# Kernel optimization log

Hardware: AMD Instinct MI355X
Metric: run time of the kernel (lower is better)

Reference implementation:

```python
import jax, jax.numpy as jnp
import numpy as np

H = 16          # local heads
DN = 128        # qk_nope_head_dim
DR = 64         # qk_rope_head_dim
DV = 128        # v_head_dim
QL = 1536       # q_lora_rank
KVL = 512       # kv_lora_rank
HID = 5120      # hidden_size
T = 2048        # tokens
EPS = 1e-6
THETA = 10000.0
SCALE = (DN + DR) ** -0.5


def rmsnorm(x, w):
    return x * jax.lax.rsqrt(jnp.mean(x * x, axis=-1, keepdims=True) + EPS) * w


def rope_interleaved(x, pos):
    # non-neox (GPT-J interleaved) partial RoPE on last dim DR; x: [T, h, DR]
    inv_freq = 1.0 / (THETA ** (jnp.arange(0, DR, 2, dtype=jnp.float32) / DR))
    freqs = pos[:, None].astype(jnp.float32) * inv_freq          # [T, DR/2]
    cos = jnp.cos(freqs)[:, None, :]
    sin = jnp.sin(freqs)[:, None, :]
    x1, x2 = x[..., 0::2], x[..., 1::2]
    o1 = x1 * cos - x2 * sin
    o2 = x2 * cos + x1 * sin
    return jnp.stack([o1, o2], axis=-1).reshape(x.shape)


def setup_inputs() -> dict:
    key = jax.random.key(0)
    ks = jax.random.split(key, 8)
    s = lambda d: 1.0 / np.sqrt(d)
    return {
        "positions": jnp.arange(T, dtype=jnp.int64),
        "hidden_states": jax.random.normal(ks[0], (T, HID), jnp.float32),
        "wq_a": jax.random.normal(ks[1], (HID, QL), jnp.float32) * s(HID),
        "q_a_ln": jnp.ones((QL,), jnp.float32),
        "wq_b": jax.random.normal(ks[2], (QL, H * (DN + DR)), jnp.float32) * s(QL),
        "wkv_a": jax.random.normal(ks[3], (HID, KVL + DR), jnp.float32) * s(HID),
        "kv_a_ln": jnp.ones((KVL,), jnp.float32),
        "wkv_b": jax.random.normal(ks[4], (KVL, H * (DN + DV)), jnp.float32) * s(KVL),
        "wo": jax.random.normal(ks[5], (H * DV, HID), jnp.float32) * s(H * DV),
    }


def reference(positions, hidden_states, wq_a, q_a_ln, wq_b, wkv_a, kv_a_ln, wkv_b, wo):
    Tn = hidden_states.shape[0]
    # Q path: low-rank down, RMSNorm, up to per-head qk dims
    q = rmsnorm(hidden_states @ wq_a, q_a_ln) @ wq_b            # [T, H*(DN+DR)]
    q = q.reshape(Tn, H, DN + DR)
    q_nope, q_pe = q[..., :DN], q[..., DN:]
    # KV path: joint down-projection -> latent + shared rope key
    kv = hidden_states @ wkv_a                                   # [T, KVL+DR]
    c_kv, k_pe = kv[:, :KVL], kv[:, KVL:]
    c_kv = rmsnorm(c_kv, kv_a_ln)
    kvb = (c_kv @ wkv_b).reshape(Tn, H, DN + DV)
    k_nope, v = kvb[..., :DN], kvb[..., DN:]
    # partial RoPE on rope sub-dims only
    q_pe = rope_interleaved(q_pe, positions)                     # [T, H, DR]
    k_pe = rope_interleaved(k_pe[:, None, :], positions)         # [T, 1, DR]
    # causal attention over full qk_head_dim
    scores = (jnp.einsum('thd,shd->hts', q_nope, k_nope)
              + jnp.einsum('thd,sod->hts', q_pe, k_pe)) * SCALE  # [H, T, T]
    mask = jnp.tril(jnp.ones((Tn, Tn), bool))
    scores = jnp.where(mask[None], scores, jnp.finfo(scores.dtype).min)
    attn = jax.nn.softmax(scores, axis=-1)
    out = jnp.einsum('hts,shd->thd', attn, v).reshape(Tn, H * DV)
    return out @ wo                                              # [T, HID]
```

## Files before the change

### kernel.cpp

```cpp
#include <hip/hip_runtime.h>
#include <hip/hip_bf16.h>


typedef __attribute__((ext_vector_type(8))) short bf16x8;
typedef __attribute__((ext_vector_type(4))) float f32x4;

#define T_SEQ 2048
#define NH 16
#define DNOPE 128
#define DROPE 64
#define DVAL 128
#define QLORA 1536
#define KVLORA 512
#define HID 5120
#define ATTN_SCALE 0.07216878364870323f

static __device__ __forceinline__ float bf2f(__hip_bfloat16 b) { return __bfloat162float(b); }

__global__ void cvt_kernel(const float* __restrict__ in, __hip_bfloat16* __restrict__ out, int n) {
  for (int i = (blockIdx.x * 256 + threadIdx.x) * 4; i < n; i += gridDim.x * 256 * 4) {
    float4 v = *(const float4*)(in + i);
    out[i + 0] = __float2bfloat16(v.x);
    out[i + 1] = __float2bfloat16(v.y);
    out[i + 2] = __float2bfloat16(v.z);
    out[i + 3] = __float2bfloat16(v.w);
  }
}

__global__ void transpose_cvt_kernel(const float* __restrict__ in, __hip_bfloat16* __restrict__ out,
                                     int R, int C) {
  __shared__ float tile[32][33];
  int bi = blockIdx.x, bj = blockIdx.y;
  int tx = threadIdx.x & 31, ty = threadIdx.x >> 5;
#pragma unroll
  for (int k2 = 0; k2 < 4; k2++) {
    int r = bi * 32 + ty + k2 * 8;
    tile[ty + k2 * 8][tx] = in[(size_t)r * C + bj * 32 + tx];
  }
  __syncthreads();
#pragma unroll
  for (int k2 = 0; k2 < 4; k2++) {
    int cc = bj * 32 + ty + k2 * 8;
    out[(size_t)cc * R + bi * 32 + tx] = __float2bfloat16(tile[tx][ty + k2 * 8]);
  }
}

__global__ void rmsnorm_kernel(const float* __restrict__ in, int in_stride, int cols,
                               const float* __restrict__ wgt,
                               __hip_bfloat16* __restrict__ out, int out_stride) {
  int row = blockIdx.x;
  const float* x = in + (size_t)row * in_stride;
  float ss = 0.f;
  for (int c = threadIdx.x; c < cols; c += 256) { float v = x[c]; ss += v * v; }
#pragma unroll
  for (int d = 1; d < 64; d <<= 1) ss += __shfl_xor(ss, d, 64);
  __shared__ float red[4];
  if ((threadIdx.x & 63) == 0) red[threadIdx.x >> 6] = ss;
  __syncthreads();
  float tot = red[0] + red[1] + red[2] + red[3];
  float r = rsqrtf(tot / cols + 1e-6f);
  __hip_bfloat16* o = out + (size_t)row * out_stride;
  for (int c = threadIdx.x; c < cols; c += 256)
    o[c] = __float2bfloat16(x[c] * r * wgt[c]);
}

__global__ void rope_q_kernel(__hip_bfloat16* __restrict__ q) {
  int row = blockIdx.x;
#pragma unroll
  for (int jj = 0; jj < 2; jj++) {
    int v = threadIdx.x + 256 * jj;
    int h = v >> 5, i = v & 31;
    float inv = powf(10000.f, -(2.f * i) / 64.f);
    float fr = (float)row * inv;
    float s, c;
    sincosf(fr, &s, &c);
    __hip_bfloat16* p = q + (size_t)row * 3072 + h * 192 + 128 + 2 * i;
    float x1 = bf2f(p[0]), x2 = bf2f(p[1]);
    p[0] = __float2bfloat16(x1 * c - x2 * s);
    p[1] = __float2bfloat16(x2 * c + x1 * s);
  }
}

__global__ void rope_k_kernel(const float* __restrict__ kv, __hip_bfloat16* __restrict__ kpe) {
  int row = blockIdx.x;
  int i = threadIdx.x;
  if (i < 32) {
    float inv = powf(10000.f, -(2.f * i) / 64.f);
    float fr = (float)row * inv;
    float s, c;
    sincosf(fr, &s, &c);
    float x1 = kv[(size_t)row * 576 + 512 + 2 * i];
    float x2 = kv[(size_t)row * 576 + 513 + 2 * i];
    kpe[(size_t)row * 64 + 2 * i]     = __float2bfloat16(x1 * c - x2 * s);
    kpe[(size_t)row * 64 + 2 * i + 1] = __float2bfloat16(x2 * c + x1 * s);
  }
}

#define BT_PAD 40
template <bool OUT_BF16>
__global__ __launch_bounds__(256, 2) void gemm_bt_kernel(
    const __hip_bfloat16* __restrict__ A, const __hip_bfloat16* __restrict__ Bt,
    void* __restrict__ Cout, int M, int N, int K) {
  __shared__ __hip_bfloat16 As[2][128][BT_PAD];
  __shared__ __hip_bfloat16 Bs[2][128][BT_PAD];
  const int t = threadIdx.x;
  const int w = t >> 6, l = t & 63;
  const int lr = l & 15, lh = l >> 4;
  const int wr = w >> 1, wc = w & 1;
  const int bm = blockIdx.x, bn = blockIdx.y;

  const int arow = t >> 1;
  const int ak = (t & 1) * 16;
  const __hip_bfloat16* Aptr = A + (size_t)(bm * 128 + arow) * K + ak;
  int brow = bn * 128 + arow;
  if (brow >= N) brow = N - 1;
  const __hip_bfloat16* Bptr = Bt + (size_t)brow * K + ak;

  f32x4 acc[4][4];
#pragma unroll
  for (int i = 0; i < 4; i++)
#pragma unroll
    for (int j = 0; j < 4; j++) acc[i][j] = f32x4{0.f, 0.f, 0.f, 0.f};

  const int KT = K >> 5;
  bf16x8 ra0, ra1, rb0, rb1;
  ra0 = *(const bf16x8*)(Aptr);
  ra1 = *(const bf16x8*)(Aptr + 8);
  rb0 = *(const bf16x8*)(Bptr);
  rb1 = *(const bf16x8*)(Bptr + 8);
  *(bf16x8*)&As[0][arow][ak] = ra0;
  *(bf16x8*)&As[0][arow][ak + 8] = ra1;
  *(bf16x8*)&Bs[0][arow][ak] = rb0;
  *(bf16x8*)&Bs[0][arow][ak + 8] = rb1;

  int cur = 0;
  for (int kt = 0; kt < KT; ++kt) {
    if (kt + 1 < KT) {
      const __hip_bfloat16* ap = Aptr + (kt + 1) * 32;
      const __hip_bfloat16* bp = Bptr + (kt + 1) * 32;
      ra0 = *(const bf16x8*)(ap);
      ra1 = *(const bf16x8*)(ap + 8);
      rb0 = *(const bf16x8*)(bp);
      rb1 = *(const bf16x8*)(bp + 8);
    }
    __syncthreads();
    bf16x8 af[4], bff[4];
#pragma unroll
    for (int m = 0; m < 4; m++) af[m] = *(bf16x8*)&As[cur][wr * 64 + m * 16 + lr][lh * 8];
#pragma unroll
    for (int n = 0; n < 4; n++) bff[n] = *(bf16x8*)&Bs[cur][wc * 64 + n * 16 + lr][lh * 8];
#pragma unroll
    for (int m = 0; m < 4; m++)
#pragma unroll
      for (int n = 0; n < 4; n++)
        acc[m][n] = __builtin_amdgcn_mfma_f32_16x16x32_bf16(af[m], bff[n], acc[m][n], 0, 0, 0);
    __syncthreads();
    if (kt + 1 < KT) {
      int nb = cur ^ 1;
      *(bf16x8*)&As[nb][arow][ak] = ra0;
      *(bf16x8*)&As[nb][arow][ak + 8] = ra1;
      *(bf16x8*)&Bs[nb][arow][ak] = rb0;
      *(bf16x8*)&Bs[nb][arow][ak + 8] = rb1;
      cur = nb;
    }
  }
#pragma unroll
  for (int m = 0; m < 4; m++) {
    int row = bm * 128 + wr * 64 + m * 16 + lh * 4;
#pragma unroll
    for (int n = 0; n < 4; n++) {
      int col = bn * 128 + wc * 64 + n * 16 + lr;
      if (col < N) {
#pragma unroll
        for (int j = 0; j < 4; j++) {
          if (OUT_BF16)
            ((__hip_bfloat16*)Cout)[(size_t)(row + j) * N + col] = __float2bfloat16(acc[m][n][j]);
          else
            ((float*)Cout)[(size_t)(row + j) * N + col] = acc[m][n][j];
        }
      }
    }
  }
}

__global__ __launch_bounds__(256, 2) void attn_kernel(
    const __hip_bfloat16* __restrict__ Q, const __hip_bfloat16* __restrict__ KVB,
    const __hip_bfloat16* __restrict__ KPE, __hip_bfloat16* __restrict__ Out) {
  __shared__ __hip_bfloat16 Ks[64][200];
  __shared__ __hip_bfloat16 Vs[128][72];
  __shared__ __hip_bfloat16 Ps[4][16][72];

  const int t = threadIdx.x;
  const int w = t >> 6, l = t & 63;
  const int lr = l & 15, lh = l >> 4;
  const int bm = (int)gridDim.x - 1 - (int)blockIdx.x;
  const int h = blockIdx.y;

  bf16x8 aq[6];
  const int qrow = bm * 64 + w * 16 + lr;
  const __hip_bfloat16* qp = Q + (size_t)qrow * 3072 + h * 192 + lh * 8;
#pragma unroll
  for (int ks = 0; ks < 6; ks++) aq[ks] = *(const bf16x8*)(qp + ks * 32);

  f32x4 o_acc[8];
#pragma unroll
  for (int i = 0; i < 8; i++) o_acc[i] = f32x4{0.f, 0.f, 0.f, 0.f};
  float m_run[4], l_run[4];
#pragma unroll
  for (int j = 0; j < 4; j++) { m_run[j] = -INFINITY; l_run[j] = 0.f; }

  for (int kb = 0; kb <= bm; ++kb) {
    const int s0 = kb * 64;
#pragma unroll
    for (int j = 0; j < 6; j++) {
      int c = t + 256 * j;
      int row = c / 24;
      int col8 = (c % 24) * 8;
      const __hip_bfloat16* src;
      if (col8 < 128) src = KVB + (size_t)(s0 + row) * 4096 + h * 256 + col8;
      else            src = KPE + (size_t)(s0 + row) * 64 + (col8 - 128);
      *(bf16x8*)&Ks[row][col8] = *(const bf16x8*)src;
    }
#pragma unroll
    for (int j = 0; j < 4; j++) {
      int c = t + 256 * j;
      int srow = c >> 4;
      int dv8 = (c & 15) * 8;
      bf16x8 v = *(const bf16x8*)(KVB + (size_t)(s0 + srow) * 4096 + h * 256 + 128 + dv8);
      int sc = srow >> 3, sl = srow & 7;
#pragma unroll
      for (int i = 0; i < 8; i++) {
        int dv = dv8 + i;
        Vs[dv][((sc ^ ((dv >> 3) & 7)) << 3) | sl] = ((__hip_bfloat16*)&v)[i];
      }
    }
    __syncthreads();

    f32x4 sa[4];
#pragma unroll
    for (int nf = 0; nf < 4; nf++) sa[nf] = f32x4{0.f, 0.f, 0.f, 0.f};
#pragma unroll
    for (int ks = 0; ks < 6; ks++) {
#pragma unroll
      for (int nf = 0; nf < 4; nf++) {
        bf16x8 b = *(bf16x8*)&Ks[nf * 16 + lr][ks * 32 + lh * 8];
        sa[nf] = __builtin_amdgcn_mfma_f32_16x16x32_bf16(aq[ks], b, sa[nf], 0, 0, 0);
      }
    }
    float sv[4][4];
    const bool diag = (kb == bm);
#pragma unroll
    for (int nf = 0; nf < 4; nf++) {
      int scol = s0 + nf * 16 + lr;
#pragma unroll
      for (int j = 0; j < 4; j++) {
        float x = sa[nf][j] * ATTN_SCALE;
        if (diag) {
          int qr = bm * 64 + w * 16 + lh * 4 + j;
          if (scol > qr) x = -1e30f;
        }
        sv[nf][j] = x;
      }
    }
    float pm[4], fac[4];
#pragma unroll
    for (int j = 0; j < 4; j++) {
      float mx = fmaxf(fmaxf(sv[0][j], sv[1][j]), fmaxf(sv[2][j], sv[3][j]));
#pragma unroll
      for (int d = 1; d < 16; d <<= 1) mx = fmaxf(mx, __shfl_xor(mx, d, 64));
      float mn = fmaxf(m_run[j], mx);
      fac[j] = __expf(m_run[j] - mn);
      m_run[j] = mn;
      pm[j] = mn;
    }
    float rs[4] = {0.f, 0.f, 0.f, 0.f};
#pragma unroll
    for (int nf = 0; nf < 4; nf++) {
#pragma unroll
      for (int j = 0; j < 4; j++) {
        float p = __expf(sv[nf][j] - pm[j]);
        rs[j] += p;
        Ps[w][lh * 4 + j][nf * 16 + lr] = __float2bfloat16(p);
      }
    }
#pragma unroll
    for (int j = 0; j < 4; j++) {
      float s = rs[j];
#pragma unroll
      for (int d = 1; d < 16; d <<= 1) s += __shfl_xor(s, d, 64);
      l_run[j] = l_run[j] * fac[j] + s;
    }
#pragma unroll
    for (int nf = 0; nf < 8; nf++)
#pragma unroll
      for (int j = 0; j < 4; j++) o_acc[nf][j] *= fac[j];

#pragma unroll
    for (int ks = 0; ks < 2; ks++) {
      bf16x8 pa = *(bf16x8*)&Ps[w][lr][ks * 32 + lh * 8];
#pragma unroll
      for (int nf = 0; nf < 8; nf++) {
        int dv = nf * 16 + lr;
        int c8 = ks * 4 + lh;
        bf16x8 vb = *(bf16x8*)&Vs[dv][((c8 ^ ((dv >> 3) & 7)) << 3)];
        o_acc[nf] = __builtin_amdgcn_mfma_f32_16x16x32_bf16(pa, vb, o_acc[nf], 0, 0, 0);
      }
    }
    __syncthreads();
  }
#pragma unroll
  for (int nf = 0; nf < 8; nf++) {
    int col = h * 128 + nf * 16 + lr;
#pragma unroll
    for (int j = 0; j < 4; j++) {
      int row = bm * 64 + w * 16 + lh * 4 + j;
      Out[(size_t)row * 2048 + col] = __float2bfloat16(o_acc[nf][j] / l_run[j]);
    }
  }
}

extern "C" void kernel_launch(void* const* d_in, const int* in_sizes, int n_in,
                              void* d_out, int out_size, void* d_ws, size_t ws_size,
                              hipStream_t stream) {
  const float* hidden  = (const float*)d_in[1];
  const float* wq_a    = (const float*)d_in[2];
  const float* q_a_ln  = (const float*)d_in[3];
  const float* wq_b    = (const float*)d_in[4];
  const float* wkv_a   = (const float*)d_in[5];
  const float* kv_a_ln = (const float*)d_in[6];
  const float* wkv_b   = (const float*)d_in[7];
  const float* wo      = (const float*)d_in[8];
  float* out = (float*)d_out;

  char* ws = (char*)d_ws;
  size_t off = 0;
  auto alloc = [&](size_t bytes) { void* p = ws + off; off += (bytes + 255) & ~(size_t)255; return p; };
  __hip_bfloat16* h_bf    = (__hip_bfloat16*)alloc((size_t)2048 * 5120 * 2);
  __hip_bfloat16* wq_a_t  = (__hip_bfloat16*)alloc((size_t)1536 * 5120 * 2);
  __hip_bfloat16* wq_b_t  = (__hip_bfloat16*)alloc((size_t)3072 * 1536 * 2);
  __hip_bfloat16* wkv_a_t = (__hip_bfloat16*)alloc((size_t)576 * 5120 * 2);
  __hip_bfloat16* wkv_b_t = (__hip_bfloat16*)alloc((size_t)4096 * 512 * 2);
  __hip_bfloat16* wo_t    = (__hip_bfloat16*)alloc((size_t)5120 * 2048 * 2);
  float*          q_lat   = (float*)alloc((size_t)2048 * 1536 * 4);
  float*          kv_f    = (float*)alloc((size_t)2048 * 576 * 4);
  __hip_bfloat16* q_a_bf  = (__hip_bfloat16*)alloc((size_t)2048 * 1536 * 2);
  __hip_bfloat16* ckv_bf  = (__hip_bfloat16*)alloc((size_t)2048 * 512 * 2);
  __hip_bfloat16* kpe_bf  = (__hip_bfloat16*)alloc((size_t)2048 * 64 * 2);
  __hip_bfloat16* q_bf    = (__hip_bfloat16*)alloc((size_t)2048 * 3072 * 2);
  __hip_bfloat16* kvb_bf  = (__hip_bfloat16*)alloc((size_t)2048 * 4096 * 2);
  __hip_bfloat16* attn_o  = (__hip_bfloat16*)alloc((size_t)2048 * 2048 * 2);
  (void)ws_size; (void)in_sizes; (void)n_in; (void)out_size;

  cvt_kernel<<<1024, 256, 0, stream>>>(hidden, h_bf, 2048 * 5120);
  transpose_cvt_kernel<<<dim3(5120 / 32, 1536 / 32), 256, 0, stream>>>(wq_a, wq_a_t, 5120, 1536);
  transpose_cvt_kernel<<<dim3(1536 / 32, 3072 / 32), 256, 0, stream>>>(wq_b, wq_b_t, 1536, 3072);
  transpose_cvt_kernel<<<dim3(5120 / 32, 576 / 32), 256, 0, stream>>>(wkv_a, wkv_a_t, 5120, 576);
  transpose_cvt_kernel<<<dim3(512 / 32, 4096 / 32), 256, 0, stream>>>(wkv_b, wkv_b_t, 512, 4096);
  transpose_cvt_kernel<<<dim3(2048 / 32, 5120 / 32), 256, 0, stream>>>(wo, wo_t, 2048, 5120);

  gemm_bt_kernel<false><<<dim3(16, 12), 256, 0, stream>>>(h_bf, wq_a_t, q_lat, 2048, 1536, 5120);
  gemm_bt_kernel<false><<<dim3(16, 5), 256, 0, stream>>>(h_bf, wkv_a_t, kv_f, 2048, 576, 5120);

  rmsnorm_kernel<<<2048, 256, 0, stream>>>(q_lat, 1536, 1536, q_a_ln, q_a_bf, 1536);
  rmsnorm_kernel<<<2048, 256, 0, stream>>>(kv_f, 576, 512, kv_a_ln, ckv_bf, 512);
  rope_k_kernel<<<2048, 64, 0, stream>>>(kv_f, kpe_bf);

  gemm_bt_kernel<true><<<dim3(16, 24), 256, 0, stream>>>(q_a_bf, wq_b_t, q_bf, 2048, 3072, 1536);
  rope_q_kernel<<<2048, 256, 0, stream>>>(q_bf);

  gemm_bt_kernel<true><<<dim3(16, 32), 256, 0, stream>>>(ckv_bf, wkv_b_t, kvb_bf, 2048, 4096, 512);

  attn_kernel<<<dim3(32, 16), 256, 0, stream>>>(q_bf, kvb_bf, kpe_bf, attn_o);

  gemm_bt_kernel<false><<<dim3(16, 40), 256, 0, stream>>>(attn_o, wo_t, out, 2048, 5120, 2048);
}
```

Baseline: 619.0 us.

## Use direct global-to-LDS loads in GEMM and fuse q/kv down-projections

The GEMM kernel now stages tiles with global_load_lds directly into unpadded shared memory, uses one barrier per K step, and raises wave priority around the MFMA block. The wq_a and wkv_a weights are transposed into one concatenated matrix so a single GEMM produces both latents. The rmsnorm and rope_k kernels read from the strided combined buffer. This removes register staging and a barrier, and cuts one launch while improving grid fill. Removing the LDS padding may introduce bank conflicts on fragment reads.

```diff
diff --git a/kernel.cpp b/kernel.cpp
--- a/kernel.cpp
+++ b/kernel.cpp
@@ -1,18 +1,12 @@
 #include <hip/hip_runtime.h>
 #include <hip/hip_bf16.h>
 
-
 typedef __attribute__((ext_vector_type(8))) short bf16x8;
 typedef __attribute__((ext_vector_type(4))) float f32x4;
 
-#define T_SEQ 2048
-#define NH 16
-#define DNOPE 128
-#define DROPE 64
-#define DVAL 128
-#define QLORA 1536
-#define KVLORA 512
-#define HID 5120
+typedef __attribute__((address_space(1))) const unsigned int gu32;
+typedef __attribute__((address_space(3))) unsigned int lu32;
+
 #define ATTN_SCALE 0.07216878364870323f
 
 static __device__ __forceinline__ float bf2f(__hip_bfloat16 b) { return __bfloat162float(b); }
@@ -81,7 +75,8 @@
   }
 }
 
-__global__ void rope_k_kernel(const float* __restrict__ kv, __hip_bfloat16* __restrict__ kpe) {
+__global__ void rope_k_kernel(const float* __restrict__ src, int stride,
+                              __hip_bfloat16* __restrict__ kpe) {
   int row = blockIdx.x;
   int i = threadIdx.x;
   if (i < 32) {
@@ -89,32 +84,35 @@
     float fr = (float)row * inv;
     float s, c;
     sincosf(fr, &s, &c);
-    float x1 = kv[(size_t)row * 576 + 512 + 2 * i];
-    float x2 = kv[(size_t)row * 576 + 513 + 2 * i];
+    float x1 = src[(size_t)row * stride + 2 * i];
+    float x2 = src[(size_t)row * stride + 2 * i + 1];
     kpe[(size_t)row * 64 + 2 * i]     = __float2bfloat16(x1 * c - x2 * s);
     kpe[(size_t)row * 64 + 2 * i + 1] = __float2bfloat16(x2 * c + x1 * s);
   }
 }
 
-#define BT_PAD 40
 template <bool OUT_BF16>
-__global__ __launch_bounds__(256, 2) void gemm_bt_kernel(
+__global__ __launch_bounds__(256, 2) void gemm_lds_kernel(
     const __hip_bfloat16* __restrict__ A, const __hip_bfloat16* __restrict__ Bt,
     void* __restrict__ Cout, int M, int N, int K) {
-  __shared__ __hip_bfloat16 As[2][128][BT_PAD];
-  __shared__ __hip_bfloat16 Bs[2][128][BT_PAD];
+  __shared__ __hip_bfloat16 As[2][128][32];
+  __shared__ __hip_bfloat16 Bs[2][128][32];
   const int t = threadIdx.x;
   const int w = t >> 6, l = t & 63;
   const int lr = l & 15, lh = l >> 4;
   const int wr = w >> 1, wc = w & 1;
   const int bm = blockIdx.x, bn = blockIdx.y;
 
-  const int arow = t >> 1;
-  const int ak = (t & 1) * 16;
-  const __hip_bfloat16* Aptr = A + (size_t)(bm * 128 + arow) * K + ak;
-  int brow = bn * 128 + arow;
-  if (brow >= N) brow = N - 1;
-  const __hip_bfloat16* Bptr = Bt + (size_t)brow * K + ak;
+  const int r0 = l >> 2;
+  const int c0 = (l & 3) * 8;
+  const int rowA0 = w * 16 + r0;
+  const int rowA1 = (4 + w) * 16 + r0;
+  const __hip_bfloat16* Ag0 = A + (size_t)(bm * 128 + rowA0) * K + c0;
+  const __hip_bfloat16* Ag1 = A + (size_t)(bm * 128 + rowA1) * K + c0;
+  int br0 = bn * 128 + rowA0; if (br0 >= N) br0 = N - 1;
+  int br1 = bn * 128 + rowA1; if (br1 >= N) br1 = N - 1;
+  const __hip_bfloat16* Bg0 = Bt + (size_t)br0 * K + c0;
+  const __hip_bfloat16* Bg1 = Bt + (size_t)br1 * K + c0;
 
   f32x4 acc[4][4];
 #pragma unroll
@@ -122,47 +120,33 @@
 #pragma unroll
     for (int j = 0; j < 4; j++) acc[i][j] = f32x4{0.f, 0.f, 0.f, 0.f};
 
+  auto issue = [&](int kt, int buf) {
+    const int ko = kt * 32;
+    __builtin_amdgcn_global_load_lds((gu32*)(Ag0 + ko), (lu32*)&As[buf][rowA0][c0], 16, 0, 0);
+    __builtin_amdgcn_global_load_lds((gu32*)(Ag1 + ko), (lu32*)&As[buf][rowA1][c0], 16, 0, 0);
+    __builtin_amdgcn_global_load_lds((gu32*)(Bg0 + ko), (lu32*)&Bs[buf][rowA0][c0], 16, 0, 0);
+    __builtin_amdgcn_global_load_lds((gu32*)(Bg1 + ko), (lu32*)&Bs[buf][rowA1][c0], 16, 0, 0);
+  };
+
   const int KT = K >> 5;
-  bf16x8 ra0, ra1, rb0, rb1;
-  ra0 = *(const bf16x8*)(Aptr);
-  ra1 = *(const bf16x8*)(Aptr + 8);
-  rb0 = *(const bf16x8*)(Bptr);
-  rb1 = *(const bf16x8*)(Bptr + 8);
-  *(bf16x8*)&As[0][arow][ak] = ra0;
-  *(bf16x8*)&As[0][arow][ak + 8] = ra1;
-  *(bf16x8*)&Bs[0][arow][ak] = rb0;
-  *(bf16x8*)&Bs[0][arow][ak + 8] = rb1;
-
+  issue(0, 0);
   int cur = 0;
   for (int kt = 0; kt < KT; ++kt) {
-    if (kt + 1 < KT) {
-      const __hip_bfloat16* ap = Aptr + (kt + 1) * 32;
-      const __hip_bfloat16* bp = Bptr + (kt + 1) * 32;
-      ra0 = *(const bf16x8*)(ap);
-      ra1 = *(const bf16x8*)(ap + 8);
-      rb0 = *(const bf16x8*)(bp);
-      rb1 = *(const bf16x8*)(bp + 8);
-    }
     __syncthreads();
+    if (kt + 1 < KT) issue(kt + 1, cur ^ 1);
     bf16x8 af[4], bff[4];
 #pragma unroll
     for (int m = 0; m < 4; m++) af[m] = *(bf16x8*)&As[cur][wr * 64 + m * 16 + lr][lh * 8];
 #pragma unroll
     for (int n = 0; n < 4; n++) bff[n] = *(bf16x8*)&Bs[cur][wc * 64 + n * 16 + lr][lh * 8];
+    __builtin_amdgcn_s_setprio(1);
 #pragma unroll
     for (int m = 0; m < 4; m++)
 #pragma unroll
       for (int n = 0; n < 4; n++)
         acc[m][n] = __builtin_amdgcn_mfma_f32_16x16x32_bf16(af[m], bff[n], acc[m][n], 0, 0, 0);
-    __syncthreads();
-    if (kt + 1 < KT) {
-      int nb = cur ^ 1;
-      *(bf16x8*)&As[nb][arow][ak] = ra0;
-      *(bf16x8*)&As[nb][arow][ak + 8] = ra1;
-      *(bf16x8*)&Bs[nb][arow][ak] = rb0;
-      *(bf16x8*)&Bs[nb][arow][ak + 8] = rb1;
-      cur = nb;
-    }
+    __builtin_amdgcn_s_setprio(0);
+    cur ^= 1;
   }
 #pragma unroll
   for (int m = 0; m < 4; m++) {
@@ -336,13 +320,11 @@
   size_t off = 0;
   auto alloc = [&](size_t bytes) { void* p = ws + off; off += (bytes + 255) & ~(size_t)255; return p; };
   __hip_bfloat16* h_bf    = (__hip_bfloat16*)alloc((size_t)2048 * 5120 * 2);
-  __hip_bfloat16* wq_a_t  = (__hip_bfloat16*)alloc((size_t)1536 * 5120 * 2);
+  __hip_bfloat16* qkvw_t  = (__hip_bfloat16*)alloc((size_t)2112 * 5120 * 2);
   __hip_bfloat16* wq_b_t  = (__hip_bfloat16*)alloc((size_t)3072 * 1536 * 2);
-  __hip_bfloat16* wkv_a_t = (__hip_bfloat16*)alloc((size_t)576 * 5120 * 2);
   __hip_bfloat16* wkv_b_t = (__hip_bfloat16*)alloc((size_t)4096 * 512 * 2);
   __hip_bfloat16* wo_t    = (__hip_bfloat16*)alloc((size_t)5120 * 2048 * 2);
-  float*          q_lat   = (float*)alloc((size_t)2048 * 1536 * 4);
-  float*          kv_f    = (float*)alloc((size_t)2048 * 576 * 4);
+  float*          qkv_lat = (float*)alloc((size_t)2048 * 2112 * 4);
   __hip_bfloat16* q_a_bf  = (__hip_bfloat16*)alloc((size_t)2048 * 1536 * 2);
   __hip_bfloat16* ckv_bf  = (__hip_bfloat16*)alloc((size_t)2048 * 512 * 2);
   __hip_bfloat16* kpe_bf  = (__hip_bfloat16*)alloc((size_t)2048 * 64 * 2);
@@ -352,25 +334,24 @@
   (void)ws_size; (void)in_sizes; (void)n_in; (void)out_size;
 
   cvt_kernel<<<1024, 256, 0, stream>>>(hidden, h_bf, 2048 * 5120);
-  transpose_cvt_kernel<<<dim3(5120 / 32, 1536 / 32), 256, 0, stream>>>(wq_a, wq_a_t, 5120, 1536);
-  transpose_cvt_kernel<<<dim3(1536 / 32, 3072 / 32), 256, 0, stream>>>(wq_b, wq_b_t, 1536, 3072);
-  transpose_cvt_kernel<<<dim3(5120 / 32, 576 / 32), 256, 0, stream>>>(wkv_a, wkv_a_t, 5120, 576);
-  transpose_cvt_kernel<<<dim3(512 / 32, 4096 / 32), 256, 0, stream>>>(wkv_b, wkv_b_t, 512, 4096);
-  transpose_cvt_kernel<<<dim3(2048 / 32, 5120 / 32), 256, 0, stream>>>(wo, wo_t, 2048, 5120);
-
-  gemm_bt_kernel<false><<<dim3(16, 12), 256, 0, stream>>>(h_bf, wq_a_t, q_lat, 2048, 1536, 5120);
-  gemm_bt_kernel<false><<<dim3(16, 5), 256, 0, stream>>>(h_bf, wkv_a_t, kv_f, 2048, 576, 5120);
-
-  rmsnorm_kernel<<<2048, 256, 0, stream>>>(q_lat, 1536, 1536, q_a_ln, q_a_bf, 1536);
-  rmsnorm_kernel<<<2048, 256, 0, stream>>>(kv_f, 576, 512, kv_a_ln, ckv_bf, 512);
-  rope_k_kernel<<<2048, 64, 0, stream>>>(kv_f, kpe_bf);
-
-  gemm_bt_kernel<true><<<dim3(16, 24), 256, 0, stream>>>(q_a_bf, wq_b_t, q_bf, 2048, 3072, 1536);
+  transpose_cvt_kernel<<<dim3(160, 48), 256, 0, stream>>>(wq_a, qkvw_t, 5120, 1536);
+  transpose_cvt_kernel<<<dim3(160, 18), 256, 0, stream>>>(wkv_a, qkvw_t + (size_t)1536 * 5120, 5120, 576);
+  transpose_cvt_kernel<<<dim3(48, 96), 256, 0, stream>>>(wq_b, wq_b_t, 1536, 3072);
+  transpose_cvt_kernel<<<dim3(16, 128), 256, 0, stream>>>(wkv_b, wkv_b_t, 512, 4096);
+  transpose_cvt_kernel<<<dim3(64, 160), 256, 0, stream>>>(wo, wo_t, 2048, 5120);
+
+  gemm_lds_kernel<false><<<dim3(16, 17), 256, 0, stream>>>(h_bf, qkvw_t, qkv_lat, 2048, 2112, 5120);
+
+  rmsnorm_kernel<<<2048, 256, 0, stream>>>(qkv_lat, 2112, 1536, q_a_ln, q_a_bf, 1536);
+  rmsnorm_kernel<<<2048, 256, 0, stream>>>(qkv_lat + 1536, 2112, 512, kv_a_ln, ckv_bf, 512);
+  rope_k_kernel<<<2048, 64, 0, stream>>>(qkv_lat + 2048, 2112, kpe_bf);
+
+  gemm_lds_kernel<true><<<dim3(16, 24), 256, 0, stream>>>(q_a_bf, wq_b_t, q_bf, 2048, 3072, 1536);
   rope_q_kernel<<<2048, 256, 0, stream>>>(q_bf);
 
-  gemm_bt_kernel<true><<<dim3(16, 32), 256, 0, stream>>>(ckv_bf, wkv_b_t, kvb_bf, 2048, 4096, 512);
+  gemm_lds_kernel<true><<<dim3(16, 32), 256, 0, stream>>>(ckv_bf, wkv_b_t, kvb_bf, 2048, 4096, 512);
 
   attn_kernel<<<dim3(32, 16), 256, 0, stream>>>(q_bf, kvb_bf, kpe_bf, attn_o);
 
-  gemm_bt_kernel<false><<<dim3(16, 40), 256, 0, stream>>>(attn_o, wo_t, out, 2048, 5120, 2048);
-}
+  gemm_lds_kernel<false><<<dim3(16, 40), 256, 0, stream>>>(attn_o, wo_t, out, 2048, 5120, 2048);
+}
```

Measured after the change: 547.9 us. 1.13x faster.
